# Performance work log

Hardware: AMD Instinct MI355X
Metric: run time of the kernel (lower is better)

Reference implementation:

```python
import jax, jax.numpy as jnp
import numpy as np

B, L, D, H = 2, 1024, 1024, 16
HD = D // H  # 64


def _skew(x):
    # x: (BH, L, 2L-1) -> (BH, L, L); Music-Transformer skew trick.
    BH, Lx, _ = x.shape
    x = jnp.pad(x, ((0, 0), (0, 0), (1, 0)))            # (BH, L, 2L)
    x = x.reshape(BH, 2 * Lx * Lx)                        # flatten
    x = jnp.pad(x, ((0, 0), (0, Lx - 1)))                 # append L-1 zeros
    x = x.reshape(BH, Lx + 1, 2 * Lx - 1)
    return x[:, :Lx, Lx - 1:]


def setup_inputs() -> dict:
    key = jax.random.key(0)
    ks = jax.random.split(key, 10)
    s = 1.0 / np.sqrt(D)
    return {
        "x": jax.random.normal(ks[0], (B, L, D), jnp.float32),
        "Wq": jax.random.normal(ks[1], (D, D), jnp.float32) * s,
        "bq": jnp.zeros((D,), jnp.float32),
        "Wk": jax.random.normal(ks[2], (D, D), jnp.float32) * s,
        "bk": jnp.zeros((D,), jnp.float32),
        "Wv": jax.random.normal(ks[3], (D, D), jnp.float32) * s,
        "bv": jnp.zeros((D,), jnp.float32),
        "Wo": jax.random.normal(ks[4], (D, D), jnp.float32) * s,
        "bo": jnp.zeros((D,), jnp.float32),
        "rel_pos_emb": jax.random.normal(ks[5], (2 * L - 1, HD), jnp.float32),
    }


def reference(x, Wq, bq, Wk, bk, Wv, bv, Wo, bo, rel_pos_emb):
    Bx, Lx, Dx = x.shape
    hd = Dx // H
    scale = hd ** (-0.5)
    # projections (torch Linear: x @ W.T + b)
    q = (x @ Wq.T + bq).reshape(Bx, Lx, H, hd).transpose(0, 2, 1, 3)  # (B,H,L,hd)
    k = (x @ Wk.T + bk).reshape(Bx, Lx, H, hd).transpose(0, 2, 1, 3)
    v = (x @ Wv.T + bv).reshape(Bx, Lx, H, hd).transpose(0, 2, 1, 3)
    scores = jnp.einsum('bhid,bhjd->bhij', q, k)                      # (B,H,L,L)
    rel = jnp.einsum('bhid,rd->bhir', q, rel_pos_emb)                 # (B,H,L,2L-1)
    rel = _skew(rel.reshape(Bx * H, Lx, 2 * Lx - 1)).reshape(Bx, H, Lx, Lx)
    attn = jax.nn.softmax((scores + rel) * scale, axis=-1)
    ctx = jnp.einsum('bhij,bhjd->bhid', attn, v)                      # (B,H,L,hd)
    ctx = ctx.transpose(0, 2, 1, 3).reshape(Bx, Lx, Dx)
    return ctx @ Wo.T + bo
```

## Files before the change

### kernel.cpp

```cpp
#include <hip/hip_runtime.h>
#include <hip/hip_bf16.h>

typedef __bf16 bf16_t;
typedef __bf16 bf16x8 __attribute__((ext_vector_type(8)));
typedef __bf16 bf16x4 __attribute__((ext_vector_type(4)));
typedef float f32x4 __attribute__((ext_vector_type(4)));

#define B_ 2
#define L_ 1024
#define D_ 1024
#define H_ 16
#define HD_ 64

__global__ __launch_bounds__(256) void cast_kernel(const float* __restrict__ src,
                                                   bf16_t* __restrict__ dst,
                                                   int n4) {
    int i = blockIdx.x * 256 + threadIdx.x;
    if (i < n4) {
        const float4 v = ((const float4*)src)[i];
        bf16x4 o;
        o[0] = (bf16_t)v.x; o[1] = (bf16_t)v.y;
        o[2] = (bf16_t)v.z; o[3] = (bf16_t)v.w;
        ((bf16x4*)dst)[i] = o;
    }
}

__global__ __launch_bounds__(256) void cast4_kernel(
    const float* __restrict__ s0, const float* __restrict__ s1,
    const float* __restrict__ s2, const float* __restrict__ s3,
    bf16_t* __restrict__ d0, bf16_t* __restrict__ d1,
    bf16_t* __restrict__ d2, bf16_t* __restrict__ d3, int n4) {
    const int z = blockIdx.y;
    const float* src = (z == 0) ? s0 : (z == 1) ? s1 : (z == 2) ? s2 : s3;
    bf16_t* dst = (z == 0) ? d0 : (z == 1) ? d1 : (z == 2) ? d2 : d3;
    int i = blockIdx.x * 256 + threadIdx.x;
    if (i < n4) {
        const float4 v = ((const float4*)src)[i];
        bf16x4 o;
        o[0] = (bf16_t)v.x; o[1] = (bf16_t)v.y;
        o[2] = (bf16_t)v.z; o[3] = (bf16_t)v.w;
        ((bf16x4*)dst)[i] = o;
    }
}

__global__ __launch_bounds__(256) void conv_e_kernel(const float* __restrict__ E,
                                                     bf16_t* __restrict__ Eb) {
    int idx = blockIdx.x * 256 + threadIdx.x;
    if (idx < 64) Eb[idx] = (bf16_t)0.f;
    if (idx < 2047 * 64) Eb[64 + idx] = (bf16_t)E[idx];
}

__global__ __launch_bounds__(256) void qkv_gemm_kernel(
    const bf16_t* __restrict__ xb,
    const bf16_t* __restrict__ Wqb, const bf16_t* __restrict__ Wkb,
    const bf16_t* __restrict__ Wvb,
    const float* __restrict__ bq, const float* __restrict__ bk2,
    const float* __restrict__ bv2,
    bf16_t* __restrict__ qbh, bf16_t* __restrict__ kbh,
    bf16_t* __restrict__ vtb) {
    constexpr int K = D_;
    __shared__ __align__(16) bf16_t As[64][72];
    __shared__ __align__(16) bf16_t Bs[64][72];

    const int z = blockIdx.z;
    const bf16_t* W = (z == 0) ? Wqb : (z == 1) ? Wkb : Wvb;
    const float* bias = (z == 0) ? bq : (z == 1) ? bk2 : bv2;
    const float alpha = (z == 0) ? 0.125f : 1.0f;

    const int tid = threadIdx.x;
    const int m0 = blockIdx.y * 64;
    const int n0 = blockIdx.x * 64;
    const int wave = tid >> 6;
    const int lane = tid & 63;
    const int wm = (wave >> 1) << 5;
    const int wn = (wave & 1) << 5;
    const int lrow = lane & 15;
    const int quad = lane >> 4;
    const int r0 = tid >> 3;
    const int c8 = (tid & 7) << 3;

    f32x4 acc[2][2] = {};

    for (int k0 = 0; k0 < K; k0 += 64) {
        *(uint4*)&As[r0][c8]      = *(const uint4*)&xb[(size_t)(m0 + r0) * K + k0 + c8];
        *(uint4*)&As[r0 + 32][c8] = *(const uint4*)&xb[(size_t)(m0 + r0 + 32) * K + k0 + c8];
        *(uint4*)&Bs[r0][c8]      = *(const uint4*)&W[(size_t)(n0 + r0) * K + k0 + c8];
        *(uint4*)&Bs[r0 + 32][c8] = *(const uint4*)&W[(size_t)(n0 + r0 + 32) * K + k0 + c8];
        __syncthreads();

#pragma unroll
        for (int kc = 0; kc < 2; ++kc) {
            bf16x8 af[2], bfr[2];
            af[0]  = *(const bf16x8*)&As[wm + lrow][kc * 32 + 8 * quad];
            af[1]  = *(const bf16x8*)&As[wm + 16 + lrow][kc * 32 + 8 * quad];
            bfr[0] = *(const bf16x8*)&Bs[wn + lrow][kc * 32 + 8 * quad];
            bfr[1] = *(const bf16x8*)&Bs[wn + 16 + lrow][kc * 32 + 8 * quad];
#pragma unroll
            for (int t = 0; t < 2; ++t)
#pragma unroll
                for (int u = 0; u < 2; ++u)
                    acc[t][u] = __builtin_amdgcn_mfma_f32_16x16x32_bf16(
                        af[t], bfr[u], acc[t][u], 0, 0, 0);
        }
        __syncthreads();
    }

#pragma unroll
    for (int t = 0; t < 2; ++t) {
#pragma unroll
        for (int u = 0; u < 2; ++u) {
            const int col = n0 + wn + u * 16 + lrow;
            const float bvv = bias[col];
            const int h = col >> 6, d = col & 63;
            if (z < 2) {
                bf16_t* outp = z ? kbh : qbh;
#pragma unroll
                for (int r = 0; r < 4; ++r) {
                    const int row = m0 + wm + t * 16 + quad * 4 + r;
                    const int b = row >> 10, i = row & 1023;
                    outp[((size_t)((b * H_ + h) * L_ + i)) * HD_ + d] =
                        (bf16_t)((acc[t][u][r] + bvv) * alpha);
                }
            } else {
                const int row0 = m0 + wm + t * 16 + quad * 4;
                const int b = row0 >> 10, i = row0 & 1023;
                bf16x4 pk;
#pragma unroll
                for (int r = 0; r < 4; ++r) pk[r] = (bf16_t)(acc[t][u][r] + bvv);
                *(bf16x4*)&vtb[((size_t)((b * H_ + h) * HD_ + d)) * L_ + i] = pk;
            }
        }
    }
}

__global__ __launch_bounds__(256) void out_gemm_kernel(
    const bf16_t* __restrict__ A, const bf16_t* __restrict__ W,
    const float* __restrict__ bias, float* __restrict__ outF) {
    constexpr int K = D_;
    __shared__ __align__(16) bf16_t As[64][72];
    __shared__ __align__(16) bf16_t Bs[64][72];

    const int tid = threadIdx.x;
    const int m0 = blockIdx.y * 64;
    const int n0 = blockIdx.x * 64;
    const int wave = tid >> 6;
    const int lane = tid & 63;
    const int wm = (wave >> 1) << 5;
    const int wn = (wave & 1) << 5;
    const int lrow = lane & 15;
    const int quad = lane >> 4;
    const int r0 = tid >> 3;
    const int c8 = (tid & 7) << 3;

    f32x4 acc[2][2] = {};

    for (int k0 = 0; k0 < K; k0 += 64) {
        *(uint4*)&As[r0][c8]      = *(const uint4*)&A[(size_t)(m0 + r0) * K + k0 + c8];
        *(uint4*)&As[r0 + 32][c8] = *(const uint4*)&A[(size_t)(m0 + r0 + 32) * K + k0 + c8];
        *(uint4*)&Bs[r0][c8]      = *(const uint4*)&W[(size_t)(n0 + r0) * K + k0 + c8];
        *(uint4*)&Bs[r0 + 32][c8] = *(const uint4*)&W[(size_t)(n0 + r0 + 32) * K + k0 + c8];
        __syncthreads();

#pragma unroll
        for (int kc = 0; kc < 2; ++kc) {
            bf16x8 af[2], bfr[2];
            af[0]  = *(const bf16x8*)&As[wm + lrow][kc * 32 + 8 * quad];
            af[1]  = *(const bf16x8*)&As[wm + 16 + lrow][kc * 32 + 8 * quad];
            bfr[0] = *(const bf16x8*)&Bs[wn + lrow][kc * 32 + 8 * quad];
            bfr[1] = *(const bf16x8*)&Bs[wn + 16 + lrow][kc * 32 + 8 * quad];
#pragma unroll
            for (int t = 0; t < 2; ++t)
#pragma unroll
                for (int u = 0; u < 2; ++u)
                    acc[t][u] = __builtin_amdgcn_mfma_f32_16x16x32_bf16(
                        af[t], bfr[u], acc[t][u], 0, 0, 0);
        }
        __syncthreads();
    }

#pragma unroll
    for (int t = 0; t < 2; ++t) {
#pragma unroll
        for (int u = 0; u < 2; ++u) {
            const int col = n0 + wn + u * 16 + lrow;
            const float bvv = bias[col];
#pragma unroll
            for (int r = 0; r < 4; ++r) {
                const int row = m0 + wm + t * 16 + quad * 4 + r;
                outF[(size_t)row * D_ + col] = acc[t][u][r] + bvv;
            }
        }
    }
}

__global__ __launch_bounds__(256) void fattn_kernel(
    const bf16_t* __restrict__ qbh, const bf16_t* __restrict__ kbh,
    const bf16_t* __restrict__ vtb, const bf16_t* __restrict__ Eb,
    bf16_t* __restrict__ ctx) {
    __shared__ __align__(16) char smem[33792];
    bf16_t (*RP)[32][104] = (bf16_t(*)[32][104])smem;
    float  (*Om)[32][64]  = (float(*)[32][64])smem;
    float  (*ml)[32][2]   = (float(*)[32][2])(smem + 32768);

    const int tid = threadIdx.x;
    const int w = tid >> 6;
    const int lane = tid & 63;
    const int q4 = lane >> 4;
    const int n = lane & 15;
    const int bh = blockIdx.y;
    const int b = bh >> 4;
    const int h = bh & 15;
    const int ib = blockIdx.x * 32;

    bf16x8 aq[2][2];
#pragma unroll
    for (int m = 0; m < 2; ++m) {
        const bf16x8* qrow =
            (const bf16x8*)(qbh + ((size_t)bh * L_ + ib + 16 * m + n) * HD_);
        aq[m][0] = qrow[q4];
        aq[m][1] = qrow[4 + q4];
    }

    const bf16_t* vbase = vtb + (size_t)bh * HD_ * L_;

    f32x4 o[2][4] = {};
    float m_r[2][4], l_r[2][4];
#pragma unroll
    for (int m = 0; m < 2; ++m)
#pragma unroll
        for (int r = 0; r < 4; ++r) { m_r[m][r] = -1e30f; l_r[m][r] = 0.f; }

    for (int t = 0; t < 4; ++t) {
        const int j0 = w * 256 + t * 64;

        f32x4 s[2][4] = {};
#pragma unroll
        for (int u = 0; u < 4; ++u) {
#pragma unroll
            for (int kc = 0; kc < 2; ++kc) {
                const bf16x8 bk = *(const bf16x8*)(kbh +
                    ((size_t)bh * L_ + j0 + 16 * u + n) * HD_ + kc * 32 + 8 * q4);
#pragma unroll
                for (int m = 0; m < 2; ++m)
                    s[m][u] = __builtin_amdgcn_mfma_f32_16x16x32_bf16(
                        aq[m][kc], bk, s[m][u], 0, 0, 0);
            }
        }

        const int rbase = j0 - ib + 992;
#pragma unroll
        for (int up = 0; up < 6; ++up) {
            f32x4 rc[2] = {};
#pragma unroll
            for (int kc = 0; kc < 2; ++kc) {
                const bf16x8 be = *(const bf16x8*)(Eb +
                    ((size_t)(rbase + 16 * up + n)) * HD_ + kc * 32 + 8 * q4);
#pragma unroll
                for (int m = 0; m < 2; ++m)
                    rc[m] = __builtin_amdgcn_mfma_f32_16x16x32_bf16(
                        aq[m][kc], be, rc[m], 0, 0, 0);
            }
#pragma unroll
            for (int m = 0; m < 2; ++m)
#pragma unroll
                for (int r = 0; r < 4; ++r)
                    RP[w][16 * m + 4 * q4 + r][16 * up + n] = (bf16_t)rc[m][r];
        }

#pragma unroll
        for (int m = 0; m < 2; ++m)
#pragma unroll
            for (int u = 0; u < 4; ++u)
#pragma unroll
                for (int r = 0; r < 4; ++r) {
                    const int row = 16 * m + 4 * q4 + r;
                    s[m][u][r] += (float)RP[w][row][16 * u + n - row + 31];
                }

#pragma unroll
        for (int m = 0; m < 2; ++m) {
#pragma unroll
            for (int r = 0; r < 4; ++r) {
                float mt = fmaxf(fmaxf(s[m][0][r], s[m][1][r]),
                                 fmaxf(s[m][2][r], s[m][3][r]));
                mt = fmaxf(mt, __shfl_xor(mt, 1));
                mt = fmaxf(mt, __shfl_xor(mt, 2));
                mt = fmaxf(mt, __shfl_xor(mt, 4));
                mt = fmaxf(mt, __shfl_xor(mt, 8));
                const float mn = fmaxf(m_r[m][r], mt);
                const float al = __expf(m_r[m][r] - mn);
                m_r[m][r] = mn;
                float ps = 0.f;
#pragma unroll
                for (int u = 0; u < 4; ++u) {
                    const float pv = __expf(s[m][u][r] - mn);
                    s[m][u][r] = pv;
                    ps += pv;
                }
                ps += __shfl_xor(ps, 1);
                ps += __shfl_xor(ps, 2);
                ps += __shfl_xor(ps, 4);
                ps += __shfl_xor(ps, 8);
                l_r[m][r] = l_r[m][r] * al + ps;
#pragma unroll
                for (int u = 0; u < 4; ++u) o[m][u][r] *= al;
            }
        }

#pragma unroll
        for (int m = 0; m < 2; ++m)
#pragma unroll
            for (int u = 0; u < 4; ++u)
#pragma unroll
                for (int r = 0; r < 4; ++r)
                    RP[w][16 * m + 4 * q4 + r][16 * u + n] = (bf16_t)s[m][u][r];

        bf16x8 pa[2][2];
#pragma unroll
        for (int m = 0; m < 2; ++m) {
            pa[m][0] = *(const bf16x8*)&RP[w][16 * m + n][8 * q4];
            pa[m][1] = *(const bf16x8*)&RP[w][16 * m + n][32 + 8 * q4];
        }

#pragma unroll
        for (int u = 0; u < 4; ++u) {
#pragma unroll
            for (int kc = 0; kc < 2; ++kc) {
                const bf16x8 bv = *(const bf16x8*)(vbase +
                    ((size_t)(16 * u + n)) * L_ + j0 + kc * 32 + 8 * q4);
#pragma unroll
                for (int m = 0; m < 2; ++m)
                    o[m][u] = __builtin_amdgcn_mfma_f32_16x16x32_bf16(
                        pa[m][kc], bv, o[m][u], 0, 0, 0);
            }
        }
    }

    __syncthreads();
#pragma unroll
    for (int m = 0; m < 2; ++m)
#pragma unroll
        for (int u = 0; u < 4; ++u)
#pragma unroll
            for (int r = 0; r < 4; ++r)
                Om[w][16 * m + 4 * q4 + r][16 * u + n] = o[m][u][r];
    if (n == 0) {
#pragma unroll
        for (int m = 0; m < 2; ++m)
#pragma unroll
            for (int r = 0; r < 4; ++r) {
                ml[w][16 * m + 4 * q4 + r][0] = m_r[m][r];
                ml[w][16 * m + 4 * q4 + r][1] = l_r[m][r];
            }
    }
    __syncthreads();

    {
        const int row = tid >> 3;
        const int c0 = (tid & 7) * 8;
        const float m0v = ml[0][row][0], m1v = ml[1][row][0];
        const float m2v = ml[2][row][0], m3v = ml[3][row][0];
        const float ms = fmaxf(fmaxf(m0v, m1v), fmaxf(m2v, m3v));
        const float a0 = __expf(m0v - ms), a1 = __expf(m1v - ms);
        const float a2 = __expf(m2v - ms), a3 = __expf(m3v - ms);
        const float inv = 1.f / (a0 * ml[0][row][1] + a1 * ml[1][row][1] +
                                 a2 * ml[2][row][1] + a3 * ml[3][row][1]);
        bf16_t* dst = ctx + ((size_t)(b * L_ + ib + row)) * D_ + h * HD_ + c0;
#pragma unroll
        for (int cc = 0; cc < 8; ++cc) {
            const int col = c0 + cc;
            const float val = (a0 * Om[0][row][col] + a1 * Om[1][row][col] +
                               a2 * Om[2][row][col] + a3 * Om[3][row][col]) * inv;
            dst[cc] = (bf16_t)val;
        }
    }
}

extern "C" void kernel_launch(void* const* d_in, const int* in_sizes, int n_in,
                              void* d_out, int out_size, void* d_ws,
                              size_t ws_size, hipStream_t stream) {
    const float* x   = (const float*)d_in[0];
    const float* Wq  = (const float*)d_in[1];
    const float* bq  = (const float*)d_in[2];
    const float* Wk  = (const float*)d_in[3];
    const float* bk  = (const float*)d_in[4];
    const float* Wv  = (const float*)d_in[5];
    const float* bv  = (const float*)d_in[6];
    const float* Wo  = (const float*)d_in[7];
    const float* bo  = (const float*)d_in[8];
    const float* E   = (const float*)d_in[9];
    float* out = (float*)d_out;

    char* ws = (char*)d_ws;
    const size_t MB = 1024u * 1024u;
    bf16_t* xb   = (bf16_t*)(ws);
    bf16_t* Wqb  = (bf16_t*)(ws + 4 * MB);
    bf16_t* Wkb  = (bf16_t*)(ws + 6 * MB);
    bf16_t* Wvb  = (bf16_t*)(ws + 8 * MB);
    bf16_t* Wob  = (bf16_t*)(ws + 10 * MB);
    bf16_t* qbh  = (bf16_t*)(ws + 12 * MB);
    bf16_t* kbh  = (bf16_t*)(ws + 16 * MB);
    bf16_t* vtb  = (bf16_t*)(ws + 20 * MB);
    bf16_t* ctxb = (bf16_t*)(ws + 24 * MB);
    bf16_t* Eb   = (bf16_t*)(ws + 28 * MB);

    conv_e_kernel<<<512, 256, 0, stream>>>(E, Eb);
    cast_kernel<<<2048, 256, 0, stream>>>(x, xb, (B_ * L_ * D_) / 4);
    dim3 gc(1024, 4);
    cast4_kernel<<<gc, 256, 0, stream>>>(Wq, Wk, Wv, Wo, Wqb, Wkb, Wvb, Wob,
                                         (D_ * D_) / 4);

    dim3 gq(D_ / 64, (B_ * L_) / 64, 3);
    qkv_gemm_kernel<<<gq, 256, 0, stream>>>(xb, Wqb, Wkb, Wvb, bq, bk, bv,
                                            qbh, kbh, vtb);

    dim3 ga(L_ / 32, B_ * H_);
    fattn_kernel<<<ga, 256, 0, stream>>>(qbh, kbh, vtb, Eb, ctxb);

    dim3 gg(D_ / 64, (B_ * L_) / 64);
    out_gemm_kernel<<<gg, 256, 0, stream>>>(ctxb, Wob, bo, out);
}
```

Baseline: 210.1 us.

## Merge prep casts, prefetch GEMM tiles in registers, hoist attention K/V loads

Merges the three cast/convert launches into a single prep kernel, so two kernel launches are no longer paid. Both GEMMs now prefetch the next K-tile from global memory into registers before the barrier, overlapping load latency with the MFMA work. In the attention kernel, K and V fragments are loaded early, ahead of the rel-pos MFMAs and softmax, to hide global latency, and the rel band is stored transposed with packed bf16x4 writes. The cost is higher register pressure, which may lower occupancy.

After: 194.0 us. 1.08x faster.

```diff
diff --git a/kernel.cpp b/kernel.cpp
--- a/kernel.cpp
+++ b/kernel.cpp
@@ -12,42 +12,38 @@
 #define H_ 16
 #define HD_ 64
 
-__global__ __launch_bounds__(256) void cast_kernel(const float* __restrict__ src,
-                                                   bf16_t* __restrict__ dst,
-                                                   int n4) {
-    int i = blockIdx.x * 256 + threadIdx.x;
-    if (i < n4) {
+__global__ __launch_bounds__(256) void prep_kernel(
+    const float* __restrict__ x,
+    const float* __restrict__ Wq, const float* __restrict__ Wk,
+    const float* __restrict__ Wv, const float* __restrict__ Wo,
+    const float* __restrict__ E,
+    bf16_t* __restrict__ xb,
+    bf16_t* __restrict__ Wqb, bf16_t* __restrict__ Wkb,
+    bf16_t* __restrict__ Wvb, bf16_t* __restrict__ Wob,
+    bf16_t* __restrict__ Eb) {
+    const int bid = blockIdx.x;
+    if (bid < 6144) {
+        const float* src;
+        bf16_t* dst;
+        int i;
+        if (bid < 2048) {
+            src = x; dst = xb; i = bid * 256 + threadIdx.x;
+        } else {
+            const int z = (bid - 2048) >> 10;
+            src = (z == 0) ? Wq : (z == 1) ? Wk : (z == 2) ? Wv : Wo;
+            dst = (z == 0) ? Wqb : (z == 1) ? Wkb : (z == 2) ? Wvb : Wob;
+            i = ((bid - 2048) & 1023) * 256 + threadIdx.x;
+        }
         const float4 v = ((const float4*)src)[i];
         bf16x4 o;
         o[0] = (bf16_t)v.x; o[1] = (bf16_t)v.y;
         o[2] = (bf16_t)v.z; o[3] = (bf16_t)v.w;
         ((bf16x4*)dst)[i] = o;
-    }
-}
-
-__global__ __launch_bounds__(256) void cast4_kernel(
-    const float* __restrict__ s0, const float* __restrict__ s1,
-    const float* __restrict__ s2, const float* __restrict__ s3,
-    bf16_t* __restrict__ d0, bf16_t* __restrict__ d1,
-    bf16_t* __restrict__ d2, bf16_t* __restrict__ d3, int n4) {
-    const int z = blockIdx.y;
-    const float* src = (z == 0) ? s0 : (z == 1) ? s1 : (z == 2) ? s2 : s3;
-    bf16_t* dst = (z == 0) ? d0 : (z == 1) ? d1 : (z == 2) ? d2 : d3;
-    int i = blockIdx.x * 256 + threadIdx.x;
-    if (i < n4) {
-        const float4 v = ((const float4*)src)[i];
-        bf16x4 o;
-        o[0] = (bf16_t)v.x; o[1] = (bf16_t)v.y;
-        o[2] = (bf16_t)v.z; o[3] = (bf16_t)v.w;
-        ((bf16x4*)dst)[i] = o;
-    }
-}
-
-__global__ __launch_bounds__(256) void conv_e_kernel(const float* __restrict__ E,
-                                                     bf16_t* __restrict__ Eb) {
-    int idx = blockIdx.x * 256 + threadIdx.x;
-    if (idx < 64) Eb[idx] = (bf16_t)0.f;
-    if (idx < 2047 * 64) Eb[64 + idx] = (bf16_t)E[idx];
+    } else {
+        const int idx = (bid - 6144) * 256 + threadIdx.x;
+        if (idx < 64) Eb[idx] = (bf16_t)0.f;
+        if (idx < 2047 * 64) Eb[64 + idx] = (bf16_t)E[idx];
+    }
 }
 
 __global__ __launch_bounds__(256) void qkv_gemm_kernel(
@@ -81,11 +77,21 @@
 
     f32x4 acc[2][2] = {};
 
+    uint4 pA0 = *(const uint4*)&xb[(size_t)(m0 + r0) * K + c8];
+    uint4 pA1 = *(const uint4*)&xb[(size_t)(m0 + r0 + 32) * K + c8];
+    uint4 pB0 = *(const uint4*)&W[(size_t)(n0 + r0) * K + c8];
+    uint4 pB1 = *(const uint4*)&W[(size_t)(n0 + r0 + 32) * K + c8];
+
     for (int k0 = 0; k0 < K; k0 += 64) {
-        *(uint4*)&As[r0][c8]      = *(const uint4*)&xb[(size_t)(m0 + r0) * K + k0 + c8];
-        *(uint4*)&As[r0 + 32][c8] = *(const uint4*)&xb[(size_t)(m0 + r0 + 32) * K + k0 + c8];
-        *(uint4*)&Bs[r0][c8]      = *(const uint4*)&W[(size_t)(n0 + r0) * K + k0 + c8];
-        *(uint4*)&Bs[r0 + 32][c8] = *(const uint4*)&W[(size_t)(n0 + r0 + 32) * K + k0 + c8];
+        *(uint4*)&As[r0][c8] = pA0;
+        *(uint4*)&As[r0 + 32][c8] = pA1;
+        *(uint4*)&Bs[r0][c8] = pB0;
+        *(uint4*)&Bs[r0 + 32][c8] = pB1;
+        const int kn = (k0 + 64 < K) ? k0 + 64 : k0;
+        pA0 = *(const uint4*)&xb[(size_t)(m0 + r0) * K + kn + c8];
+        pA1 = *(const uint4*)&xb[(size_t)(m0 + r0 + 32) * K + kn + c8];
+        pB0 = *(const uint4*)&W[(size_t)(n0 + r0) * K + kn + c8];
+        pB1 = *(const uint4*)&W[(size_t)(n0 + r0 + 32) * K + kn + c8];
         __syncthreads();
 
 #pragma unroll
@@ -154,11 +160,21 @@
 
     f32x4 acc[2][2] = {};
 
+    uint4 pA0 = *(const uint4*)&A[(size_t)(m0 + r0) * K + c8];
+    uint4 pA1 = *(const uint4*)&A[(size_t)(m0 + r0 + 32) * K + c8];
+    uint4 pB0 = *(const uint4*)&W[(size_t)(n0 + r0) * K + c8];
+    uint4 pB1 = *(const uint4*)&W[(size_t)(n0 + r0 + 32) * K + c8];
+
     for (int k0 = 0; k0 < K; k0 += 64) {
-        *(uint4*)&As[r0][c8]      = *(const uint4*)&A[(size_t)(m0 + r0) * K + k0 + c8];
-        *(uint4*)&As[r0 + 32][c8] = *(const uint4*)&A[(size_t)(m0 + r0 + 32) * K + k0 + c8];
-        *(uint4*)&Bs[r0][c8]      = *(const uint4*)&W[(size_t)(n0 + r0) * K + k0 + c8];
-        *(uint4*)&Bs[r0 + 32][c8] = *(const uint4*)&W[(size_t)(n0 + r0 + 32) * K + k0 + c8];
+        *(uint4*)&As[r0][c8] = pA0;
+        *(uint4*)&As[r0 + 32][c8] = pA1;
+        *(uint4*)&Bs[r0][c8] = pB0;
+        *(uint4*)&Bs[r0 + 32][c8] = pB1;
+        const int kn = (k0 + 64 < K) ? k0 + 64 : k0;
+        pA0 = *(const uint4*)&A[(size_t)(m0 + r0) * K + kn + c8];
+        pA1 = *(const uint4*)&A[(size_t)(m0 + r0 + 32) * K + kn + c8];
+        pB0 = *(const uint4*)&W[(size_t)(n0 + r0) * K + kn + c8];
+        pB1 = *(const uint4*)&W[(size_t)(n0 + r0 + 32) * K + kn + c8];
         __syncthreads();
 
 #pragma unroll
@@ -198,9 +214,8 @@
     const bf16_t* __restrict__ vtb, const bf16_t* __restrict__ Eb,
     bf16_t* __restrict__ ctx) {
     __shared__ __align__(16) char smem[33792];
-    bf16_t (*RP)[32][104] = (bf16_t(*)[32][104])smem;
-    float  (*Om)[32][64]  = (float(*)[32][64])smem;
-    float  (*ml)[32][2]   = (float(*)[32][2])(smem + 32768);
+    float (*Om)[32][64] = (float(*)[32][64])smem;
+    float (*ml)[32][2]  = (float(*)[32][2])(smem + 32768);
 
     const int tid = threadIdx.x;
     const int w = tid >> 6;
@@ -212,6 +227,9 @@
     const int h = bh & 15;
     const int ib = blockIdx.x * 32;
 
+    bf16_t* band = (bf16_t*)smem + (size_t)w * (96 * 36);
+    bf16_t* ps = band;
+
     bf16x8 aq[2][2];
 #pragma unroll
     for (int m = 0; m < 2; ++m) {
@@ -233,19 +251,13 @@
     for (int t = 0; t < 4; ++t) {
         const int j0 = w * 256 + t * 64;
 
-        f32x4 s[2][4] = {};
-#pragma unroll
-        for (int u = 0; u < 4; ++u) {
-#pragma unroll
-            for (int kc = 0; kc < 2; ++kc) {
-                const bf16x8 bk = *(const bf16x8*)(kbh +
+        bf16x8 bk[4][2];
+#pragma unroll
+        for (int u = 0; u < 4; ++u)
+#pragma unroll
+            for (int kc = 0; kc < 2; ++kc)
+                bk[u][kc] = *(const bf16x8*)(kbh +
                     ((size_t)bh * L_ + j0 + 16 * u + n) * HD_ + kc * 32 + 8 * q4);
-#pragma unroll
-                for (int m = 0; m < 2; ++m)
-                    s[m][u] = __builtin_amdgcn_mfma_f32_16x16x32_bf16(
-                        aq[m][kc], bk, s[m][u], 0, 0, 0);
-            }
-        }
 
         const int rbase = j0 - ib + 992;
 #pragma unroll
@@ -261,11 +273,31 @@
                         aq[m][kc], be, rc[m], 0, 0, 0);
             }
 #pragma unroll
-            for (int m = 0; m < 2; ++m)
-#pragma unroll
-                for (int r = 0; r < 4; ++r)
-                    RP[w][16 * m + 4 * q4 + r][16 * up + n] = (bf16_t)rc[m][r];
-        }
+            for (int m = 0; m < 2; ++m) {
+                bf16x4 pk;
+#pragma unroll
+                for (int r = 0; r < 4; ++r) pk[r] = (bf16_t)rc[m][r];
+                *(bf16x4*)&band[(size_t)(16 * up + n) * 36 + 16 * m + 4 * q4] = pk;
+            }
+        }
+
+        f32x4 s[2][4] = {};
+#pragma unroll
+        for (int u = 0; u < 4; ++u)
+#pragma unroll
+            for (int kc = 0; kc < 2; ++kc)
+#pragma unroll
+                for (int m = 0; m < 2; ++m)
+                    s[m][u] = __builtin_amdgcn_mfma_f32_16x16x32_bf16(
+                        aq[m][kc], bk[u][kc], s[m][u], 0, 0, 0);
+
+        bf16x8 vf[4][2];
+#pragma unroll
+        for (int u = 0; u < 4; ++u)
+#pragma unroll
+            for (int kc = 0; kc < 2; ++kc)
+                vf[u][kc] = *(const bf16x8*)(vbase +
+                    ((size_t)(16 * u + n)) * L_ + j0 + kc * 32 + 8 * q4);
 
 #pragma unroll
         for (int m = 0; m < 2; ++m)
@@ -274,7 +306,8 @@
 #pragma unroll
                 for (int r = 0; r < 4; ++r) {
                     const int row = 16 * m + 4 * q4 + r;
-                    s[m][u][r] += (float)RP[w][row][16 * u + n - row + 31];
+                    s[m][u][r] +=
+                        (float)band[(size_t)(16 * u + n - row + 31) * 36 + row];
                 }
 
 #pragma unroll
@@ -290,18 +323,18 @@
                 const float mn = fmaxf(m_r[m][r], mt);
                 const float al = __expf(m_r[m][r] - mn);
                 m_r[m][r] = mn;
-                float ps = 0.f;
+                float psum = 0.f;
 #pragma unroll
                 for (int u = 0; u < 4; ++u) {
                     const float pv = __expf(s[m][u][r] - mn);
                     s[m][u][r] = pv;
-                    ps += pv;
+                    psum += pv;
                 }
-                ps += __shfl_xor(ps, 1);
-                ps += __shfl_xor(ps, 2);
-                ps += __shfl_xor(ps, 4);
-                ps += __shfl_xor(ps, 8);
-                l_r[m][r] = l_r[m][r] * al + ps;
+                psum += __shfl_xor(psum, 1);
+                psum += __shfl_xor(psum, 2);
+                psum += __shfl_xor(psum, 4);
+                psum += __shfl_xor(psum, 8);
+                l_r[m][r] = l_r[m][r] * al + psum;
 #pragma unroll
                 for (int u = 0; u < 4; ++u) o[m][u][r] *= al;
             }
@@ -313,27 +346,24 @@
             for (int u = 0; u < 4; ++u)
 #pragma unroll
                 for (int r = 0; r < 4; ++r)
-                    RP[w][16 * m + 4 * q4 + r][16 * u + n] = (bf16_t)s[m][u][r];
+                    ps[(size_t)(16 * m + 4 * q4 + r) * 72 + 16 * u + n] =
+                        (bf16_t)s[m][u][r];
 
         bf16x8 pa[2][2];
 #pragma unroll
         for (int m = 0; m < 2; ++m) {
-            pa[m][0] = *(const bf16x8*)&RP[w][16 * m + n][8 * q4];
-            pa[m][1] = *(const bf16x8*)&RP[w][16 * m + n][32 + 8 * q4];
-        }
-
-#pragma unroll
-        for (int u = 0; u < 4; ++u) {
-#pragma unroll
-            for (int kc = 0; kc < 2; ++kc) {
-                const bf16x8 bv = *(const bf16x8*)(vbase +
-                    ((size_t)(16 * u + n)) * L_ + j0 + kc * 32 + 8 * q4);
+            pa[m][0] = *(const bf16x8*)&ps[(size_t)(16 * m + n) * 72 + 8 * q4];
+            pa[m][1] = *(const bf16x8*)&ps[(size_t)(16 * m + n) * 72 + 32 + 8 * q4];
+        }
+
+#pragma unroll
+        for (int u = 0; u < 4; ++u)
+#pragma unroll
+            for (int kc = 0; kc < 2; ++kc)
 #pragma unroll
                 for (int m = 0; m < 2; ++m)
                     o[m][u] = __builtin_amdgcn_mfma_f32_16x16x32_bf16(
-                        pa[m][kc], bv, o[m][u], 0, 0, 0);
-            }
-        }
+                        pa[m][kc], vf[u][kc], o[m][u], 0, 0, 0);
     }
 
     __syncthreads();
@@ -404,11 +434,8 @@
     bf16_t* ctxb = (bf16_t*)(ws + 24 * MB);
     bf16_t* Eb   = (bf16_t*)(ws + 28 * MB);
 
-    conv_e_kernel<<<512, 256, 0, stream>>>(E, Eb);
-    cast_kernel<<<2048, 256, 0, stream>>>(x, xb, (B_ * L_ * D_) / 4);
-    dim3 gc(1024, 4);
-    cast4_kernel<<<gc, 256, 0, stream>>>(Wq, Wk, Wv, Wo, Wqb, Wkb, Wvb, Wob,
-                                         (D_ * D_) / 4);
+    prep_kernel<<<6656, 256, 0, stream>>>(x, Wq, Wk, Wv, Wo, E,
+                                          xb, Wqb, Wkb, Wvb, Wob, Eb);
 
     dim3 gq(D_ / 64, (B_ * L_) / 64, 3);
     qkv_gemm_kernel<<<gq, 256, 0, stream>>>(xb, Wqb, Wkb, Wvb, bq, bk, bv,
```
